# Kernel optimization log

Measured on AMD Instinct MI355X. Metric: run time of the kernel, lower is better.

Reference implementation:

```python
import jax, jax.numpy as jnp
import numpy as np

D_MODEL = 1024
N_HEADS = 16
HEAD_DIM = D_MODEL // N_HEADS


def setup_inputs() -> dict:
    key = jax.random.key(0)
    ks = jax.random.split(key, 9)
    B, S = 2, 2048
    s = 1.0 / np.sqrt(D_MODEL)
    x = jax.random.normal(ks[0], (B, S, D_MODEL), dtype=jnp.float32)
    Wq = jax.random.normal(ks[1], (N_HEADS, D_MODEL, HEAD_DIM), dtype=jnp.float32) * s
    Wk = jax.random.normal(ks[2], (N_HEADS, D_MODEL, HEAD_DIM), dtype=jnp.float32) * s
    Wv = jax.random.normal(ks[3], (N_HEADS, D_MODEL, HEAD_DIM), dtype=jnp.float32) * s
    bq = jax.random.normal(ks[4], (N_HEADS, HEAD_DIM), dtype=jnp.float32) * s
    bk = jax.random.normal(ks[5], (N_HEADS, HEAD_DIM), dtype=jnp.float32) * s
    bv = jax.random.normal(ks[6], (N_HEADS, HEAD_DIM), dtype=jnp.float32) * s
    Wp = jax.random.normal(ks[7], (D_MODEL, D_MODEL), dtype=jnp.float32) * s
    bp = jax.random.normal(ks[8], (D_MODEL,), dtype=jnp.float32) * s
    return {"x": x, "Wq": Wq, "Wk": Wk, "Wv": Wv, "bq": bq, "bk": bk, "bv": bv, "Wp": Wp, "bp": bp}


def reference(x, Wq, Wk, Wv, bq, bk, bv, Wp, bp):
    # Per-head projections batched over heads: [B,S,D] x [H,D,E] -> [B,H,S,E]
    Q = jnp.einsum('bsd,hde->bhse', x, Wq) + bq[None, :, None, :]
    K = jnp.einsum('bsd,hde->bhse', x, Wk) + bk[None, :, None, :]
    V = jnp.einsum('bsd,hde->bhse', x, Wv) + bv[None, :, None, :]
    scores = jnp.einsum('bhse,bhte->bhst', Q, K) / jnp.sqrt(jnp.asarray(HEAD_DIM, x.dtype))
    attn = jax.nn.softmax(scores, axis=-1)          # [B,H,S,S]
    out = jnp.einsum('bhst,bhte->bhse', attn, V)    # [B,H,S,E]
    B, H, S, E = out.shape
    concat = out.transpose(0, 2, 1, 3).reshape(B, S, H * E)  # concat heads along feature
    return concat @ Wp.T + bp
```

## Files before the change

### kernel.cpp

```cpp
#include <hip/hip_runtime.h>
#include <hip/hip_bf16.h>

typedef __attribute__((ext_vector_type(8))) short short8;
typedef __attribute__((ext_vector_type(4))) float float4_t;

#define D_MODEL 1024
#define N_HEADS 16
#define HEAD_DIM 64
#define B_SZ 2
#define SEQ 2048
#define M_ROWS (B_SZ*SEQ)
#define NQKV 3072
#define SC_LOG2E 0.18033688011112042f

__device__ __forceinline__ unsigned short f2bf(float f) {
  unsigned u = __float_as_uint(f);
  u += 0x7FFFu + ((u >> 16) & 1u);
  return (unsigned short)(u >> 16);
}

__device__ __forceinline__ void gl_lds16(const unsigned short* g, unsigned short* l) {
  __builtin_amdgcn_global_load_lds(
      (const __attribute__((address_space(1))) unsigned int*)(size_t)g,
      (__attribute__((address_space(3))) unsigned int*)(unsigned int)(size_t)l,
      16, 0, 0);
}

__global__ void prep(const float* __restrict__ x, const float* __restrict__ Wp,
                     const float* __restrict__ Wq, const float* __restrict__ Wk,
                     const float* __restrict__ Wv,
                     unsigned short* __restrict__ xb, unsigned short* __restrict__ Wpb,
                     unsigned short* __restrict__ Wall) {
  __shared__ float t[16][17];
  int bid = blockIdx.x;
  if (bid < 5120) {
    const float* src; unsigned short* dst; int base;
    if (bid < 4096) { src = x;  dst = xb;  base = bid * 1024 + threadIdx.x * 4; }
    else            { src = Wp; dst = Wpb; base = (bid - 4096) * 1024 + threadIdx.x * 4; }
    float4 v = *(const float4*)(src + base);
    dst[base + 0] = f2bf(v.x);
    dst[base + 1] = f2bf(v.y);
    dst[base + 2] = f2bf(v.z);
    dst[base + 3] = f2bf(v.w);
  } else {
    int u = bid - 5120;
    int sel = u >> 12;
    u &= 4095;
    const float* W = sel == 0 ? Wq : (sel == 1 ? Wk : Wv);
    int d0 = (u & 63) * 16, e0 = ((u >> 6) & 3) * 16, hh = u >> 8;
    int tx = threadIdx.x & 15, ty = threadIdx.x >> 4;
    t[ty][tx] = W[hh * (D_MODEL * HEAD_DIM) + (d0 + ty) * HEAD_DIM + e0 + tx];
    __syncthreads();
    Wall[(size_t)(sel * 1024 + hh * 64 + e0 + ty) * D_MODEL + d0 + tx] = f2bf(t[tx][ty]);
  }
}

__global__ __launch_bounds__(256) void qkv_gemm(const unsigned short* __restrict__ xb,
                                                const unsigned short* __restrict__ Wall,
                                                const float* __restrict__ bq,
                                                const float* __restrict__ bk,
                                                const float* __restrict__ bv,
                                                unsigned short* __restrict__ Qb,
                                                unsigned short* __restrict__ Kb,
                                                unsigned short* __restrict__ Vtb) {
  __shared__ unsigned short As[128 * 32], Bs[128 * 32];
  __shared__ __align__(16) unsigned short Stage[4][16 * 72];
  const int m0 = blockIdx.x * 128, n0 = blockIdx.y * 128;
  const int lane = threadIdx.x & 63, w = threadIdx.x >> 6;
  const int l16 = lane & 15, quad = lane >> 4;
  const int wm = w & 1, wn = w >> 1;
  const int ldrow = lane >> 2, ldcol = (lane & 3) * 8;
  const unsigned short* ga0 = xb + (size_t)(m0 + w * 32 + ldrow) * D_MODEL + ldcol;
  const unsigned short* ga1 = ga0 + 16 * D_MODEL;
  const unsigned short* gb0 = Wall + (size_t)(n0 + w * 32 + ldrow) * D_MODEL + ldcol;
  const unsigned short* gb1 = gb0 + 16 * D_MODEL;
  unsigned short* lA0 = As + (w * 2 + 0) * 512;
  unsigned short* lA1 = As + (w * 2 + 1) * 512;
  unsigned short* lB0 = Bs + (w * 2 + 0) * 512;
  unsigned short* lB1 = Bs + (w * 2 + 1) * 512;
  float4_t acc[4][4];
  float4_t z = {0.f, 0.f, 0.f, 0.f};
#pragma unroll
  for (int i = 0; i < 4; i++)
#pragma unroll
    for (int j = 0; j < 4; j++) acc[i][j] = z;
  for (int k0 = 0; k0 < D_MODEL; k0 += 32) {
    __syncthreads();
    gl_lds16(ga0 + k0, lA0);
    gl_lds16(ga1 + k0, lA1);
    gl_lds16(gb0 + k0, lB0);
    gl_lds16(gb1 + k0, lB1);
    __syncthreads();
    short8 af[4], bf[4];
#pragma unroll
    for (int i = 0; i < 4; i++) af[i] = *(const short8*)&As[(wm * 64 + i * 16 + l16) * 32 + quad * 8];
#pragma unroll
    for (int j = 0; j < 4; j++) bf[j] = *(const short8*)&Bs[(wn * 64 + j * 16 + l16) * 32 + quad * 8];
#pragma unroll
    for (int i = 0; i < 4; i++)
#pragma unroll
      for (int j = 0; j < 4; j++)
        acc[i][j] = __builtin_amdgcn_mfma_f32_16x16x32_bf16(af[i], bf[j], acc[i][j], 0, 0, 0);
  }
  const int nb = n0 + wn * 64;
  const int sel = nb >> 10;
  const int h = (nb >> 6) & 15;
  const float* bias = sel == 0 ? bq : (sel == 1 ? bk : bv);
  const int mbase = m0 + wm * 64;
  const int bb = mbase >> 11;
  const size_t bh = (size_t)(bb * N_HEADS + h);
  if (sel == 2) {
    unsigned short* vs = &Stage[w][0];
    const size_t vbase = bh * (32 * 4096) + (size_t)((mbase >> 6) & 31) * 4096;
    const int e8 = lane >> 3, ch = lane & 7;
#pragma unroll
    for (int j = 0; j < 4; j++) {
      float be = bias[h * 64 + j * 16 + l16];
#pragma unroll
      for (int i = 0; i < 4; i++)
#pragma unroll
        for (int r = 0; r < 4; r++)
          vs[l16 * 72 + i * 16 + quad * 4 + r] = f2bf(acc[i][j][r] + be);
#pragma unroll
      for (int rd = 0; rd < 2; rd++) {
        int er = rd * 8 + e8;
        short8 val = *(const short8*)(vs + er * 72 + ch * 8);
        *(short8*)(Vtb + vbase + (size_t)(j * 16 + er) * 64 + ch * 8) = val;
      }
    }
  } else {
    unsigned short* st = &Stage[w][0];
    unsigned short* dst = (sel == 0) ? Qb : Kb;
    const float qsc = (sel == 0) ? SC_LOG2E : 1.0f;
    const size_t rowbase = bh * SEQ + (mbase & (SEQ - 1));
    const int r2 = lane >> 1, c2 = lane & 1;
#pragma unroll
    for (int j = 0; j < 4; j++) {
      float be = bias[h * 64 + j * 16 + l16];
#pragma unroll
      for (int i = 0; i < 4; i++)
#pragma unroll
        for (int r = 0; r < 4; r++)
          st[(i * 16 + quad * 4 + r) * 18 + l16] = f2bf((acc[i][j][r] + be) * qsc);
#pragma unroll
      for (int p = 0; p < 2; p++) {
        int row = p * 32 + r2;
        short8 val = *(const short8*)(st + row * 18 + c2 * 8);
        *(short8*)(dst + (rowbase + row) * HEAD_DIM + j * 16 + c2 * 8) = val;
      }
    }
  }
}

__global__ __launch_bounds__(256) void attn_kernel(const unsigned short* __restrict__ Q,
                                                   const unsigned short* __restrict__ K,
                                                   const unsigned short* __restrict__ Vt,
                                                   unsigned short* __restrict__ concat) {
  __shared__ __align__(16) unsigned short Ks0[64 * 72], Ks1[64 * 72];
  __shared__ __align__(16) unsigned short Vs0[64 * 72], Vs1[64 * 72];
  __shared__ __align__(16) unsigned short Ps[4][32 * 64];
  const int b = blockIdx.z, h = blockIdx.y;
  const int lane = threadIdx.x & 63, w = threadIdx.x >> 6;
  const int l16 = lane & 15, quad = lane >> 4;
  const size_t bh = (size_t)(b * N_HEADS + h);
  const int q0 = blockIdx.x * 128 + w * 32;
  float4_t z = {0.f, 0.f, 0.f, 0.f};

  short8 aq[2][2];
#pragma unroll
  for (int rg = 0; rg < 2; rg++)
#pragma unroll
    for (int hf = 0; hf < 2; hf++)
      aq[rg][hf] = *(const short8*)(Q + (bh * SEQ + q0 + rg * 16 + l16) * HEAD_DIM + hf * 32 + quad * 8);

  const int srow = lane >> 3, schk = lane & 7;
  const unsigned short* kg = K + (bh * SEQ + w * 16 + srow) * HEAD_DIM + schk * 8;
  const unsigned short* vg = Vt + bh * (32 * 4096) + (w * 16 + srow) * 64 + schk * 8;
  const int tl0 = w * 16 + srow, tl1 = tl0 + 8;
  const int kwr0 = (((tl0 >> 1) & 15) | ((tl0 & 1) << 4) | (tl0 & 32)) * 72 + schk * 8;
  const int kwr1 = (((tl1 >> 1) & 15) | ((tl1 & 1) << 4) | (tl1 & 32)) * 72 + schk * 8;
  const int vwr0 = (w * 16 + srow) * 72 + schk * 8;
  const int vwr1 = vwr0 + 8 * 72;

  float4_t o[2][4];
  float4_t ls[2] = {z, z};
#pragma unroll
  for (int rg = 0; rg < 2; rg++)
#pragma unroll
    for (int ne = 0; ne < 4; ne++) o[rg][ne] = z;
  short8 ones;
#pragma unroll
  for (int i = 0; i < 8; i++) ones[i] = (short)0x3F80;
  unsigned short* pb = &Ps[w][0];

  short8 kreg0 = *(const short8*)kg;
  short8 kreg1 = *(const short8*)(kg + 512);
  short8 vreg0 = *(const short8*)vg;
  short8 vreg1 = *(const short8*)(vg + 512);
  kg += 4096; vg += 4096;

  auto step = [&](unsigned short* kb, unsigned short* vb, int itv) {
    *(short8*)(kb + kwr0) = kreg0;
    *(short8*)(kb + kwr1) = kreg1;
    *(short8*)(vb + vwr0) = vreg0;
    *(short8*)(vb + vwr1) = vreg1;
    __syncthreads();
    if (itv < 31) {
      kreg0 = *(const short8*)kg;
      kreg1 = *(const short8*)(kg + 512);
      vreg0 = *(const short8*)vg;
      vreg1 = *(const short8*)(vg + 512);
      kg += 4096; vg += 4096;
    }
    float4_t s[2][4];
#pragma unroll
    for (int nt = 0; nt < 4; nt++) {
      short8 k0 = *(const short8*)(kb + (nt * 16 + l16) * 72 + quad * 8);
      short8 k1 = *(const short8*)(kb + (nt * 16 + l16) * 72 + 32 + quad * 8);
      s[0][nt] = __builtin_amdgcn_mfma_f32_16x16x32_bf16(aq[0][0], k0, z, 0, 0, 0);
      s[0][nt] = __builtin_amdgcn_mfma_f32_16x16x32_bf16(aq[0][1], k1, s[0][nt], 0, 0, 0);
      s[1][nt] = __builtin_amdgcn_mfma_f32_16x16x32_bf16(aq[1][0], k0, z, 0, 0, 0);
      s[1][nt] = __builtin_amdgcn_mfma_f32_16x16x32_bf16(aq[1][1], k1, s[1][nt], 0, 0, 0);
    }
#pragma unroll
    for (int rg = 0; rg < 2; rg++) {
#pragma unroll
      for (int r = 0; r < 4; r++) {
        int row = rg * 16 + quad * 4 + r;
        float p0 = __builtin_amdgcn_exp2f(s[rg][0][r]);
        float p1 = __builtin_amdgcn_exp2f(s[rg][1][r]);
        __hip_bfloat162 pp = __float22bfloat162_rn(float2{p0, p1});
        *(unsigned int*)(pb + row * 64 + 2 * l16) = *(unsigned int*)&pp;
        float p2 = __builtin_amdgcn_exp2f(s[rg][2][r]);
        float p3 = __builtin_amdgcn_exp2f(s[rg][3][r]);
        __hip_bfloat162 qq = __float22bfloat162_rn(float2{p2, p3});
        *(unsigned int*)(pb + row * 64 + 32 + 2 * l16) = *(unsigned int*)&qq;
      }
    }
    short8 pa[2][2];
#pragma unroll
    for (int rg = 0; rg < 2; rg++)
#pragma unroll
      for (int hf = 0; hf < 2; hf++)
        pa[rg][hf] = *(const short8*)(pb + (rg * 16 + l16) * 64 + hf * 32 + quad * 8);
#pragma unroll
    for (int rg = 0; rg < 2; rg++) {
      ls[rg] = __builtin_amdgcn_mfma_f32_16x16x32_bf16(pa[rg][0], ones, ls[rg], 0, 0, 0);
      ls[rg] = __builtin_amdgcn_mfma_f32_16x16x32_bf16(pa[rg][1], ones, ls[rg], 0, 0, 0);
    }
#pragma unroll
    for (int ne = 0; ne < 4; ne++) {
#pragma unroll
      for (int hf = 0; hf < 2; hf++) {
        short8 vf = *(const short8*)(vb + (ne * 16 + l16) * 72 + hf * 32 + quad * 8);
        o[0][ne] = __builtin_amdgcn_mfma_f32_16x16x32_bf16(pa[0][hf], vf, o[0][ne], 0, 0, 0);
        o[1][ne] = __builtin_amdgcn_mfma_f32_16x16x32_bf16(pa[1][hf], vf, o[1][ne], 0, 0, 0);
      }
    }
  };

  for (int it2 = 0; it2 < 16; ++it2) {
    step(Ks0, Vs0, 2 * it2);
    step(Ks1, Vs1, 2 * it2 + 1);
  }

#pragma unroll
  for (int rg = 0; rg < 2; rg++) {
#pragma unroll
    for (int r = 0; r < 4; r++) {
      float li = 1.0f / ls[rg][r];
      int sr = q0 + rg * 16 + quad * 4 + r;
#pragma unroll
      for (int ne = 0; ne < 4; ne++)
        concat[((size_t)(b * SEQ + sr)) * D_MODEL + h * 64 + ne * 16 + l16] = f2bf(o[rg][ne][r] * li);
    }
  }
}

__global__ __launch_bounds__(256) void out_gemm(const unsigned short* __restrict__ cb,
                                                const unsigned short* __restrict__ Wpb,
                                                const float* __restrict__ bp,
                                                float* __restrict__ out) {
  __shared__ unsigned short As[128 * 32], Bs[64 * 32];
  const int m0 = blockIdx.x * 128, n0 = blockIdx.y * 64;
  const int lane = threadIdx.x & 63, w = threadIdx.x >> 6;
  const int l16 = lane & 15, quad = lane >> 4;
  const int ldrow = lane >> 2, ldcol = (lane & 3) * 8;
  const unsigned short* ga0 = cb + (size_t)(m0 + w * 32 + ldrow) * D_MODEL + ldcol;
  const unsigned short* ga1 = ga0 + 16 * D_MODEL;
  const unsigned short* gb0 = Wpb + (size_t)(n0 + w * 16 + ldrow) * D_MODEL + ldcol;
  unsigned short* lA0 = As + (w * 2 + 0) * 512;
  unsigned short* lA1 = As + (w * 2 + 1) * 512;
  unsigned short* lB0 = Bs + w * 512;
  float4_t acc[2][4];
  float4_t z = {0.f, 0.f, 0.f, 0.f};
#pragma unroll
  for (int i = 0; i < 2; i++)
#pragma unroll
    for (int j = 0; j < 4; j++) acc[i][j] = z;
  for (int k0 = 0; k0 < D_MODEL; k0 += 32) {
    __syncthreads();
    gl_lds16(ga0 + k0, lA0);
    gl_lds16(ga1 + k0, lA1);
    gl_lds16(gb0 + k0, lB0);
    __syncthreads();
    short8 af[2], bf[4];
#pragma unroll
    for (int i = 0; i < 2; i++) af[i] = *(const short8*)&As[(w * 32 + i * 16 + l16) * 32 + quad * 8];
#pragma unroll
    for (int j = 0; j < 4; j++) bf[j] = *(const short8*)&Bs[(j * 16 + l16) * 32 + quad * 8];
#pragma unroll
    for (int i = 0; i < 2; i++)
#pragma unroll
      for (int j = 0; j < 4; j++)
        acc[i][j] = __builtin_amdgcn_mfma_f32_16x16x32_bf16(af[i], bf[j], acc[i][j], 0, 0, 0);
  }
#pragma unroll
  for (int i = 0; i < 2; i++)
#pragma unroll
    for (int j = 0; j < 4; j++)
#pragma unroll
      for (int r = 0; r < 4; r++) {
        int m = m0 + w * 32 + i * 16 + quad * 4 + r;
        int oc = n0 + j * 16 + l16;
        out[(size_t)m * D_MODEL + oc] = acc[i][j][r] + bp[oc];
      }
}

extern "C" void kernel_launch(void* const* d_in, const int* in_sizes, int n_in,
                              void* d_out, int out_size, void* d_ws, size_t ws_size,
                              hipStream_t stream) {
  const float* x  = (const float*)d_in[0];
  const float* Wq = (const float*)d_in[1];
  const float* Wk = (const float*)d_in[2];
  const float* Wv = (const float*)d_in[3];
  const float* bq = (const float*)d_in[4];
  const float* bk = (const float*)d_in[5];
  const float* bv = (const float*)d_in[6];
  const float* Wp = (const float*)d_in[7];
  const float* bp = (const float*)d_in[8];
  float* out = (float*)d_out;

  char* ws = (char*)d_ws;
  size_t off = 0;
  auto alloc = [&](size_t bytes) -> void* {
    void* p = ws + off;
    off += (bytes + 255) & ~(size_t)255;
    return p;
  };
  unsigned short* xb   = (unsigned short*)alloc((size_t)M_ROWS * D_MODEL * 2);
  unsigned short* Wall = (unsigned short*)alloc((size_t)NQKV * D_MODEL * 2);
  unsigned short* Wpb  = (unsigned short*)alloc((size_t)D_MODEL * D_MODEL * 2);
  unsigned short* Qb   = (unsigned short*)alloc((size_t)B_SZ * N_HEADS * SEQ * HEAD_DIM * 2);
  unsigned short* Kb   = (unsigned short*)alloc((size_t)B_SZ * N_HEADS * SEQ * HEAD_DIM * 2);
  unsigned short* Vtb  = (unsigned short*)alloc((size_t)B_SZ * N_HEADS * SEQ * HEAD_DIM * 2);
  unsigned short* cbuf = (unsigned short*)alloc((size_t)B_SZ * SEQ * D_MODEL * 2);

  prep<<<17408, 256, 0, stream>>>(x, Wp, Wq, Wk, Wv, xb, Wpb, Wall);

  qkv_gemm<<<dim3(M_ROWS / 128, NQKV / 128), 256, 0, stream>>>(xb, Wall, bq, bk, bv, Qb, Kb, Vtb);

  attn_kernel<<<dim3(SEQ / 128, N_HEADS, B_SZ), 256, 0, stream>>>(Qb, Kb, Vtb, cbuf);

  out_gemm<<<dim3(M_ROWS / 128, D_MODEL / 64), 256, 0, stream>>>(cbuf, Wpb, bp, out);
}
```

Before: 210.1 us.

## Compute transposed scores so P feeds PV MFMA from registers, drop LDS staging

The attention kernel now computes S^T (K as the A operand, Q as B), so each lane's exp'd probabilities are already laid out as the A fragment of a 16x16x16 fp16 MFMA. P therefore never round-trips through LDS, and V is stored as fp16 to match that instruction. K/V tiles are loaded straight from global memory into registers with no LDS double buffering or __syncthreads. Row sums come from per-lane accumulation plus cross-lane shuffles instead of a ones-vector MFMA. In exchange, K and V are reloaded from global or L2 by every wave without sharing through LDS, global-load latency is no longer prefetched, and fp16 P/V carries different precision and overflow behaviour than bf16.

```diff
diff --git a/kernel.cpp b/kernel.cpp
--- a/kernel.cpp
+++ b/kernel.cpp
@@ -3,6 +3,7 @@
 
 typedef __attribute__((ext_vector_type(8))) short short8;
 typedef __attribute__((ext_vector_type(4))) float float4_t;
+typedef __attribute__((ext_vector_type(4))) _Float16 half4;
 
 #define D_MODEL 1024
 #define N_HEADS 16
@@ -17,6 +18,11 @@
   unsigned u = __float_as_uint(f);
   u += 0x7FFFu + ((u >> 16) & 1u);
   return (unsigned short)(u >> 16);
+}
+
+__device__ __forceinline__ unsigned short f2h(float f) {
+  _Float16 h = (_Float16)f;
+  return *(unsigned short*)&h;
 }
 
 __device__ __forceinline__ void gl_lds16(const unsigned short* g, unsigned short* l) {
@@ -120,7 +126,7 @@
       for (int i = 0; i < 4; i++)
 #pragma unroll
         for (int r = 0; r < 4; r++)
-          vs[l16 * 72 + i * 16 + quad * 4 + r] = f2bf(acc[i][j][r] + be);
+          vs[l16 * 72 + i * 16 + quad * 4 + r] = f2h(acc[i][j][r] + be);
 #pragma unroll
       for (int rd = 0; rd < 2; rd++) {
         int er = rd * 8 + e8;
@@ -156,9 +162,6 @@
                                                    const unsigned short* __restrict__ K,
                                                    const unsigned short* __restrict__ Vt,
                                                    unsigned short* __restrict__ concat) {
-  __shared__ __align__(16) unsigned short Ks0[64 * 72], Ks1[64 * 72];
-  __shared__ __align__(16) unsigned short Vs0[64 * 72], Vs1[64 * 72];
-  __shared__ __align__(16) unsigned short Ps[4][32 * 64];
   const int b = blockIdx.z, h = blockIdx.y;
   const int lane = threadIdx.x & 63, w = threadIdx.x >> 6;
   const int l16 = lane & 15, quad = lane >> 4;
@@ -173,102 +176,64 @@
     for (int hf = 0; hf < 2; hf++)
       aq[rg][hf] = *(const short8*)(Q + (bh * SEQ + q0 + rg * 16 + l16) * HEAD_DIM + hf * 32 + quad * 8);
 
-  const int srow = lane >> 3, schk = lane & 7;
-  const unsigned short* kg = K + (bh * SEQ + w * 16 + srow) * HEAD_DIM + schk * 8;
-  const unsigned short* vg = Vt + bh * (32 * 4096) + (w * 16 + srow) * 64 + schk * 8;
-  const int tl0 = w * 16 + srow, tl1 = tl0 + 8;
-  const int kwr0 = (((tl0 >> 1) & 15) | ((tl0 & 1) << 4) | (tl0 & 32)) * 72 + schk * 8;
-  const int kwr1 = (((tl1 >> 1) & 15) | ((tl1 & 1) << 4) | (tl1 & 32)) * 72 + schk * 8;
-  const int vwr0 = (w * 16 + srow) * 72 + schk * 8;
-  const int vwr1 = vwr0 + 8 * 72;
+  const unsigned short* kbase = K + bh * SEQ * HEAD_DIM;
+  const unsigned short* vbase = Vt + bh * (32 * 4096);
 
   float4_t o[2][4];
-  float4_t ls[2] = {z, z};
 #pragma unroll
   for (int rg = 0; rg < 2; rg++)
 #pragma unroll
     for (int ne = 0; ne < 4; ne++) o[rg][ne] = z;
-  short8 ones;
-#pragma unroll
-  for (int i = 0; i < 8; i++) ones[i] = (short)0x3F80;
-  unsigned short* pb = &Ps[w][0];
-
-  short8 kreg0 = *(const short8*)kg;
-  short8 kreg1 = *(const short8*)(kg + 512);
-  short8 vreg0 = *(const short8*)vg;
-  short8 vreg1 = *(const short8*)(vg + 512);
-  kg += 4096; vg += 4096;
-
-  auto step = [&](unsigned short* kb, unsigned short* vb, int itv) {
-    *(short8*)(kb + kwr0) = kreg0;
-    *(short8*)(kb + kwr1) = kreg1;
-    *(short8*)(vb + vwr0) = vreg0;
-    *(short8*)(vb + vwr1) = vreg1;
-    __syncthreads();
-    if (itv < 31) {
-      kreg0 = *(const short8*)kg;
-      kreg1 = *(const short8*)(kg + 512);
-      vreg0 = *(const short8*)vg;
-      vreg1 = *(const short8*)(vg + 512);
-      kg += 4096; vg += 4096;
-    }
-    float4_t s[2][4];
-#pragma unroll
-    for (int nt = 0; nt < 4; nt++) {
-      short8 k0 = *(const short8*)(kb + (nt * 16 + l16) * 72 + quad * 8);
-      short8 k1 = *(const short8*)(kb + (nt * 16 + l16) * 72 + 32 + quad * 8);
-      s[0][nt] = __builtin_amdgcn_mfma_f32_16x16x32_bf16(aq[0][0], k0, z, 0, 0, 0);
-      s[0][nt] = __builtin_amdgcn_mfma_f32_16x16x32_bf16(aq[0][1], k1, s[0][nt], 0, 0, 0);
-      s[1][nt] = __builtin_amdgcn_mfma_f32_16x16x32_bf16(aq[1][0], k0, z, 0, 0, 0);
-      s[1][nt] = __builtin_amdgcn_mfma_f32_16x16x32_bf16(aq[1][1], k1, s[1][nt], 0, 0, 0);
-    }
-#pragma unroll
-    for (int rg = 0; rg < 2; rg++) {
-#pragma unroll
-      for (int r = 0; r < 4; r++) {
-        int row = rg * 16 + quad * 4 + r;
-        float p0 = __builtin_amdgcn_exp2f(s[rg][0][r]);
-        float p1 = __builtin_amdgcn_exp2f(s[rg][1][r]);
-        __hip_bfloat162 pp = __float22bfloat162_rn(float2{p0, p1});
-        *(unsigned int*)(pb + row * 64 + 2 * l16) = *(unsigned int*)&pp;
-        float p2 = __builtin_amdgcn_exp2f(s[rg][2][r]);
-        float p3 = __builtin_amdgcn_exp2f(s[rg][3][r]);
-        __hip_bfloat162 qq = __float22bfloat162_rn(float2{p2, p3});
-        *(unsigned int*)(pb + row * 64 + 32 + 2 * l16) = *(unsigned int*)&qq;
+  float lsp[2] = {0.f, 0.f};
+
+  for (int it = 0; it < 32; ++it) {
+    const unsigned short* kp = kbase + (size_t)it * 4096;
+    const unsigned short* vp = vbase + (size_t)it * 4096;
+    short8 kf[4][2];
+#pragma unroll
+    for (int tc = 0; tc < 4; tc++)
+#pragma unroll
+      for (int hf = 0; hf < 2; hf++)
+        kf[tc][hf] = *(const short8*)(kp + (tc * 16 + l16) * HEAD_DIM + hf * 32 + quad * 8);
+    half4 vf[4][4];
+#pragma unroll
+    for (int tc = 0; tc < 4; tc++)
+#pragma unroll
+      for (int ne = 0; ne < 4; ne++)
+        vf[tc][ne] = *(const half4*)(vp + (ne * 16 + l16) * 64 + tc * 16 + quad * 4);
+
+#pragma unroll
+    for (int tc = 0; tc < 4; tc++) {
+#pragma unroll
+      for (int rg = 0; rg < 2; rg++) {
+        float4_t s = __builtin_amdgcn_mfma_f32_16x16x32_bf16(kf[tc][0], aq[rg][0], z, 0, 0, 0);
+        s = __builtin_amdgcn_mfma_f32_16x16x32_bf16(kf[tc][1], aq[rg][1], s, 0, 0, 0);
+        float p0 = __builtin_amdgcn_exp2f(s[0]);
+        float p1 = __builtin_amdgcn_exp2f(s[1]);
+        float p2 = __builtin_amdgcn_exp2f(s[2]);
+        float p3 = __builtin_amdgcn_exp2f(s[3]);
+        lsp[rg] += (p0 + p1) + (p2 + p3);
+        half4 pa = {(_Float16)p0, (_Float16)p1, (_Float16)p2, (_Float16)p3};
+#pragma unroll
+        for (int ne = 0; ne < 4; ne++)
+          o[rg][ne] = __builtin_amdgcn_mfma_f32_16x16x16f16(pa, vf[tc][ne], o[rg][ne], 0, 0, 0);
       }
     }
-    short8 pa[2][2];
-#pragma unroll
-    for (int rg = 0; rg < 2; rg++)
-#pragma unroll
-      for (int hf = 0; hf < 2; hf++)
-        pa[rg][hf] = *(const short8*)(pb + (rg * 16 + l16) * 64 + hf * 32 + quad * 8);
-#pragma unroll
-    for (int rg = 0; rg < 2; rg++) {
-      ls[rg] = __builtin_amdgcn_mfma_f32_16x16x32_bf16(pa[rg][0], ones, ls[rg], 0, 0, 0);
-      ls[rg] = __builtin_amdgcn_mfma_f32_16x16x32_bf16(pa[rg][1], ones, ls[rg], 0, 0, 0);
-    }
-#pragma unroll
-    for (int ne = 0; ne < 4; ne++) {
-#pragma unroll
-      for (int hf = 0; hf < 2; hf++) {
-        short8 vf = *(const short8*)(vb + (ne * 16 + l16) * 72 + hf * 32 + quad * 8);
-        o[0][ne] = __builtin_amdgcn_mfma_f32_16x16x32_bf16(pa[0][hf], vf, o[0][ne], 0, 0, 0);
-        o[1][ne] = __builtin_amdgcn_mfma_f32_16x16x32_bf16(pa[1][hf], vf, o[1][ne], 0, 0, 0);
-      }
-    }
-  };
-
-  for (int it2 = 0; it2 < 16; ++it2) {
-    step(Ks0, Vs0, 2 * it2);
-    step(Ks1, Vs1, 2 * it2 + 1);
-  }
-
+  }
+
+  float lsf[2];
 #pragma unroll
   for (int rg = 0; rg < 2; rg++) {
+    float v = lsp[rg];
+    v += __shfl_xor(v, 16, 64);
+    v += __shfl_xor(v, 32, 64);
+    lsf[rg] = v;
+  }
+#pragma unroll
+  for (int rg = 0; rg < 2; rg++) {
 #pragma unroll
     for (int r = 0; r < 4; r++) {
-      float li = 1.0f / ls[rg][r];
+      float li = 1.0f / __shfl(lsf[rg], quad * 4 + r, 64);
       int sr = q0 + rg * 16 + quad * 4 + r;
 #pragma unroll
       for (int ne = 0; ne < 4; ne++)
```

Result: slower. 313.1 us (+49.1%).
